# Performance work log

Hardware: AMD Instinct MI355X
Metric: run time of the kernel (lower is better)

The kernel has to match this reference:

```python
import jax, jax.numpy as jnp
import numpy as np

N_NODES = 50000
N_EDGES = 1600000
D_IN = 1028
D_OUT = 256
NEG_SLOPE = 0.2


def setup_inputs() -> dict:
    key = jax.random.key(0)
    ks = jax.random.split(key, 6)
    x = jax.random.normal(ks[0], (N_NODES, D_IN), dtype=jnp.float32)
    edge_index = jax.random.randint(ks[1], (2, N_EDGES), 0, N_NODES, dtype=jnp.int64)
    # GATv2Conv params (heads=1): separate source/target linear maps, attention vector, bias
    W_l = jax.random.normal(ks[2], (D_IN, D_OUT), dtype=jnp.float32) / np.sqrt(D_IN)
    W_r = jax.random.normal(ks[3], (D_IN, D_OUT), dtype=jnp.float32) / np.sqrt(D_IN)
    att = jax.random.normal(ks[4], (D_OUT,), dtype=jnp.float32) / np.sqrt(D_OUT)
    bias = jax.random.normal(ks[5], (D_OUT,), dtype=jnp.float32) * 0.01
    return {"x": x, "edge_index": edge_index, "W_l": W_l, "W_r": W_r, "att": att, "bias": bias}


def reference(x, edge_index, W_l, W_r, att, bias):
    # Single-layer GATv2Conv(1028 -> 256, heads=1, add_self_loops=True)
    n = x.shape[0]
    xl = x @ W_l  # source-side features [N, D_OUT]
    xr = x @ W_r  # target-side features [N, D_OUT]
    loops = jnp.arange(n, dtype=edge_index.dtype)
    src = jnp.concatenate([edge_index[0], loops])  # [E + N]
    dst = jnp.concatenate([edge_index[1], loops])
    # e_ij = a . LeakyReLU(xl[j] + xr[i])
    e = jax.nn.leaky_relu(xl[src] + xr[dst], NEG_SLOPE) @ att  # [E + N]
    # softmax over incoming edges per destination node (self-loops guarantee nonempty segments)
    emax = jax.ops.segment_max(e, dst, num_segments=n)
    p = jnp.exp(e - emax[dst])
    denom = jax.ops.segment_sum(p, dst, num_segments=n)
    alpha = p / denom[dst]  # [E + N]
    out = jax.ops.segment_sum(alpha[:, None] * xl[src], dst, num_segments=n)
    return out + bias
```

## Files before the change

### kernel.cpp

```cpp
#include <hip/hip_runtime.h>
#include <hip/hip_bf16.h>
#include <stdint.h>


#define N_NODES 50000
#define N_EDGES 1600000
#define D_IN    1028
#define KPAD    1056
#define D_OUT   256
#define NB      512

#define X2B_GS     2048
#define X2B_TOT    (N_NODES * 264)
#define WT_TILES   (33 * 8)
#define HIST_GS    1024
#define PREP_BLOCKS (X2B_GS + WT_TILES + HIST_GS)
#define SCAT_GS    2048

typedef __bf16 bf16x8 __attribute__((ext_vector_type(8)));
typedef float  f32x4  __attribute__((ext_vector_type(4)));

static __device__ __forceinline__ void gl_lds16(const void* g, void* l) {
  __builtin_amdgcn_global_load_lds(
      (const __attribute__((address_space(1))) unsigned int*)g,
      (__attribute__((address_space(3))) unsigned int*)l, 16, 0, 0);
}
static __device__ __forceinline__ float bf2f(unsigned short u) {
  union { unsigned int i; float f; } c; c.i = ((unsigned int)u) << 16; return c.f;
}
static __device__ __forceinline__ unsigned short f2bf(float f) {
  union { float f; unsigned int i; } c; c.f = f;
  unsigned int r = 0x7fffu + ((c.i >> 16) & 1u);
  return (unsigned short)((c.i + r) >> 16);
}

__global__ void k_mode(const unsigned int* __restrict__ ei32, int* __restrict__ mode) {
  int t = blockIdx.x * 256 + threadIdx.x;
  if (t < 2048 && ei32[2 * t + 1] != 0u) atomicOr(mode, 1);
}

static __device__ __forceinline__ int load_idx(const int* ei, int md, int pos, int n) {
  int v = md ? ei[pos] : (int)((const long long*)ei)[pos];
  return v < 0 ? 0 : (v >= n ? n - 1 : v);
}

__global__ __launch_bounds__(256) void k_prep(const float* __restrict__ x,
    const float* __restrict__ Wl, const float* __restrict__ Wr,
    const int* __restrict__ ei, const int* __restrict__ mode,
    unsigned short* __restrict__ xb, unsigned short* __restrict__ Wt,
    int* __restrict__ deg) {
  __shared__ unsigned short tile[32][66];
  const int b = blockIdx.x, t = threadIdx.x;
  if (b < X2B_GS) {
    const int TH = X2B_GS * 256;
    for (int c = b * 256 + t; c < X2B_TOT; c += 4 * TH) {
      int cc[4], rw[4], qq[4]; float4 v[4]; bool ld[4];
#pragma unroll
      for (int u = 0; u < 4; ++u) {
        cc[u] = c + u * TH;
        ld[u] = false; rw[u] = 0; qq[u] = 0;
        if (cc[u] < X2B_TOT) {
          rw[u] = cc[u] / 264;
          qq[u] = cc[u] - rw[u] * 264;
          if (qq[u] < 257) {
            v[u] = *(const float4*)(x + (size_t)rw[u] * D_IN + 4 * qq[u]);
            ld[u] = true;
          }
        }
      }
#pragma unroll
      for (int u = 0; u < 4; ++u) {
        if (cc[u] < X2B_TOT) {
          ushort4 o = {0, 0, 0, 0};
          if (ld[u]) { o.x = f2bf(v[u].x); o.y = f2bf(v[u].y);
                       o.z = f2bf(v[u].z); o.w = f2bf(v[u].w); }
          *(ushort4*)(xb + (size_t)rw[u] * KPAD + 4 * qq[u]) = o;
        }
      }
    }
  } else if (b < X2B_GS + WT_TILES) {
    const int w = b - X2B_GS;
    const int k0 = (w >> 3) * 32, n0 = (w & 7) * 64;
#pragma unroll
    for (int j = 0; j < 8; ++j) {
      int k = 4 * j + (t >> 6), n = t & 63;
      unsigned short val = 0;
      if (k0 + k < D_IN) {
        int gn = n0 + n;
        val = f2bf(gn < D_OUT ? Wl[(size_t)(k0 + k) * D_OUT + gn]
                              : Wr[(size_t)(k0 + k) * D_OUT + (gn - D_OUT)]);
      }
      tile[k][n] = val;
    }
    __syncthreads();
#pragma unroll
    for (int j = 0; j < 8; ++j) {
      int n = 8 * j + (t >> 5), k = t & 31;
      Wt[(size_t)(n0 + n) * KPAD + k0 + k] = tile[k][n];
    }
  } else {
    const int md = *mode;
    const int TH = HIST_GS * 256;
    for (int e = (b - X2B_GS - WT_TILES) * 256 + t; e < N_EDGES; e += TH) {
      int d = load_idx(ei, md, N_EDGES + e, N_NODES);
      atomicAdd(&deg[d], 1);
    }
  }
}

__global__ __launch_bounds__(256) void k_gemm(const unsigned short* __restrict__ xb,
                                              const unsigned short* __restrict__ Wt,
                                              unsigned short* __restrict__ xf, int M) {
  __shared__ unsigned short smem[16896];
  unsigned short* As = smem;
  unsigned short* Bs = smem + 4096;
  unsigned short* Cs = smem;
  const int tid = threadIdx.x;
  const int w = tid >> 6, lane = tid & 63;
  const int m0 = blockIdx.x * 128, n0 = blockIdx.y * 128;
  const int wm = (w >> 1) * 64, wn = (w & 1) * 64;

  f32x4 zero = {0.f, 0.f, 0.f, 0.f};
  f32x4 acc[4][4];
#pragma unroll
  for (int i = 0; i < 4; ++i)
#pragma unroll
    for (int j = 0; j < 4; ++j) acc[i][j] = zero;

  const int lrow = lane >> 2, lch = lane & 3;

  for (int k0 = 0; k0 < KPAD; k0 += 32) {
    __syncthreads();
#pragma unroll
    for (int j = 0; j < 2; ++j) {
      int gm = m0 + w * 32 + j * 16 + lrow;
      if (gm >= M) gm = M - 1;
      const char* g = (const char*)xb + ((size_t)gm * KPAD + k0) * 2 + lch * 16;
      gl_lds16(g, &As[(w * 32 + j * 16) * 32]);
    }
#pragma unroll
    for (int j = 0; j < 2; ++j) {
      int gn = n0 + w * 32 + j * 16 + lrow;
      const char* g = (const char*)Wt + ((size_t)gn * KPAD + k0) * 2 + lch * 16;
      gl_lds16(g, &Bs[(w * 32 + j * 16) * 32]);
    }
    __syncthreads();

    bf16x8 af[4], bfr[4];
#pragma unroll
    for (int t = 0; t < 4; ++t)
      af[t] = *(const bf16x8*)&As[(wm + t * 16 + (lane & 15)) * 32 + (lane >> 4) * 8];
#pragma unroll
    for (int t = 0; t < 4; ++t)
      bfr[t] = *(const bf16x8*)&Bs[(wn + t * 16 + (lane & 15)) * 32 + (lane >> 4) * 8];
#pragma unroll
    for (int mt = 0; mt < 4; ++mt)
#pragma unroll
      for (int nt = 0; nt < 4; ++nt)
        acc[mt][nt] = __builtin_amdgcn_mfma_f32_16x16x32_bf16(af[mt], bfr[nt], acc[mt][nt], 0, 0, 0);
  }

  __syncthreads();
  {
    const int col = lane & 15, rq = (lane >> 4) * 4;
#pragma unroll
    for (int mt = 0; mt < 4; ++mt)
#pragma unroll
      for (int nt = 0; nt < 4; ++nt)
#pragma unroll
        for (int r = 0; r < 4; ++r)
          Cs[(wm + mt * 16 + rq + r) * 132 + wn + nt * 16 + col] = f2bf(acc[mt][nt][r]);
  }
  __syncthreads();
  {
    const int row = tid >> 1, half = tid & 1;
    int gm = m0 + row;
    if (gm < M) {
      unsigned short* dst = xf + (size_t)gm * NB + n0 + half * 64;
      const unsigned short* srcp = &Cs[row * 132 + half * 64];
#pragma unroll
      for (int j = 0; j < 8; ++j)
        *(uint4*)(dst + j * 8) = *(const uint4*)(srcp + j * 8);
    }
  }
}

__global__ __launch_bounds__(1024) void k_scan(const int* __restrict__ deg,
    int* __restrict__ rowstart, int* __restrict__ cursor, int n) {
  const int t = (int)threadIdx.x;
  const int lane = t & 63, wid = t >> 6;
  const int seg = (n + 1023) / 1024;
  const int base = t * seg;
  __shared__ int wsum[16];

  int sum = 0;
  for (int j = 0; j < seg; ++j) { int i = base + j; if (i < n) sum += deg[i]; }

  int x = sum;
#pragma unroll
  for (int off = 1; off < 64; off <<= 1) {
    int y = __shfl_up(x, off, 64);
    if (lane >= off) x += y;
  }
  if (lane == 63) wsum[wid] = x;
  __syncthreads();
  if (t < 16) {
    int v = wsum[t], s = v;
#pragma unroll
    for (int off = 1; off < 16; off <<= 1) {
      int y = __shfl_up(s, off, 16);
      if (t >= off) s += y;
    }
    wsum[t] = s - v;
  }
  __syncthreads();
  int run = wsum[wid] + (x - sum);
  for (int j = 0; j < seg; ++j) {
    int i = base + j;
    if (i < n) { rowstart[i] = run; cursor[i] = run; run += deg[i]; }
  }
  if (t == 1023) rowstart[n] = run;
}

__global__ __launch_bounds__(256) void k_scatter(const int* __restrict__ ei,
                          const int* __restrict__ mode,
                          int* __restrict__ cursor, int* __restrict__ ssrc) {
  const int md = *mode;
  const int TH = SCAT_GS * 256;
  for (int e = (int)blockIdx.x * 256 + (int)threadIdx.x; e < N_EDGES; e += TH) {
    int s = load_idx(ei, md, e, N_NODES);
    int d = load_idx(ei, md, N_EDGES + e, N_NODES);
    int pos = atomicAdd(&cursor[d], 1);
    if (pos >= 0 && pos < N_EDGES) ssrc[pos] = s;
  }
}

static __device__ __forceinline__ void unpack8(uint4 u, float* v) {
  union { unsigned int i; float f; } c;
  c.i = u.x << 16;         v[0] = c.f;
  c.i = u.x & 0xffff0000u; v[1] = c.f;
  c.i = u.y << 16;         v[2] = c.f;
  c.i = u.y & 0xffff0000u; v[3] = c.f;
  c.i = u.z << 16;         v[4] = c.f;
  c.i = u.z & 0xffff0000u; v[5] = c.f;
  c.i = u.w << 16;         v[6] = c.f;
  c.i = u.w & 0xffff0000u; v[7] = c.f;
}
static __device__ __forceinline__ float dot8(const float* v, const float* xr, const float* a) {
  float e = 0.f;
#pragma unroll
  for (int d = 0; d < 8; ++d) {
    float t = v[d] + xr[d];
    t = fmaxf(t, 0.2f * t);
    e = fmaf(a[d], t, e);
  }
  return e;
}
static __device__ __forceinline__ float red32(float e) {
#pragma unroll
  for (int off = 1; off < 32; off <<= 1) e += __shfl_xor(e, off, 64);
  return e;
}

__global__ __launch_bounds__(256) void k_gat(const unsigned short* __restrict__ xf,
    const int* __restrict__ rowstart, const int* __restrict__ ssrc,
    const float* __restrict__ att, const float* __restrict__ bias,
    float* __restrict__ out, int n) {
  const int gw = (int)blockIdx.x * 4 + (int)(threadIdx.x >> 6);
  const int lane = (int)(threadIdx.x & 63);
  const int grp = lane >> 5, gl = lane & 31;
  if (gw >= n) return;

  float a[8];
  {
    float4 A0 = ((const float4*)att)[2 * gl];
    float4 A1 = ((const float4*)att)[2 * gl + 1];
    a[0] = A0.x; a[1] = A0.y; a[2] = A0.z; a[3] = A0.w;
    a[4] = A1.x; a[5] = A1.y; a[6] = A1.z; a[7] = A1.w;
  }
  float xr[8], vs[8];
  unpack8(*(const uint4*)(xf + (size_t)gw * NB + D_OUT + 8 * gl), xr);
  unpack8(*(const uint4*)(xf + (size_t)gw * NB + 8 * gl), vs);

  float m, l, acc[8];
  {
    float e = red32(dot8(vs, xr, a));
    if (grp == 0) {
      m = e; l = 1.f;
#pragma unroll
      for (int d = 0; d < 8; ++d) acc[d] = vs[d];
    } else {
      m = -1e30f; l = 0.f;
#pragma unroll
      for (int d = 0; d < 8; ++d) acc[d] = 0.f;
    }
  }

  const int end = rowstart[gw + 1];
  int i = rowstart[gw] + grp;
  bool have = i < end;
  uint4 vu;
  if (have) {
    unsigned s = (unsigned)ssrc[i];
    vu = *(const uint4*)(xf + ((size_t)s << 9) + 8 * gl);
  }
  while (have) {
    int i2 = i + 2;
    bool have2 = i2 < end;
    uint4 vu2;
    if (have2) {
      unsigned s2 = (unsigned)ssrc[i2];
      vu2 = *(const uint4*)(xf + ((size_t)s2 << 9) + 8 * gl);
    }
    float v[8];
    unpack8(vu, v);
    float e = red32(dot8(v, xr, a));
    float mn = fmaxf(m, e);
    float sc = __expf(m - mn);
    float p  = __expf(e - mn);
#pragma unroll
    for (int d = 0; d < 8; ++d) acc[d] = fmaf(p, v[d], acc[d] * sc);
    l = fmaf(l, sc, p);
    m = mn;
    vu = vu2; i = i2; have = have2;
  }

  float mo = __shfl_xor(m, 32, 64);
  float mM = fmaxf(m, mo);
  float sA = __expf(m - mM);
  float lA = l * sA;
  float lS = lA + __shfl_xor(lA, 32, 64);
  float inv = 1.f / lS;
#pragma unroll
  for (int d = 0; d < 8; ++d) {
    float t = acc[d] * sA;
    acc[d] = t + __shfl_xor(t, 32, 64);
  }
  if (grp == 0) {
    float4 B0 = ((const float4*)bias)[2 * gl];
    float4 B1 = ((const float4*)bias)[2 * gl + 1];
    float4 o0, o1;
    o0.x = fmaf(acc[0], inv, B0.x); o0.y = fmaf(acc[1], inv, B0.y);
    o0.z = fmaf(acc[2], inv, B0.z); o0.w = fmaf(acc[3], inv, B0.w);
    o1.x = fmaf(acc[4], inv, B1.x); o1.y = fmaf(acc[5], inv, B1.y);
    o1.z = fmaf(acc[6], inv, B1.z); o1.w = fmaf(acc[7], inv, B1.w);
    ((float4*)out)[(size_t)gw * 64 + 2 * gl] = o0;
    ((float4*)out)[(size_t)gw * 64 + 2 * gl + 1] = o1;
  }
}

extern "C" void kernel_launch(void* const* d_in, const int* in_sizes, int n_in,
                              void* d_out, int out_size, void* d_ws, size_t ws_size,
                              hipStream_t stream) {
  (void)in_sizes; (void)n_in; (void)out_size; (void)ws_size;
  const float* x   = (const float*)d_in[0];
  const int*   ei  = (const int*)d_in[1];
  const float* Wl  = (const float*)d_in[2];
  const float* Wr  = (const float*)d_in[3];
  const float* att = (const float*)d_in[4];
  const float* bia = (const float*)d_in[5];
  float* out = (float*)d_out;

  const int N = N_NODES;
  const int E = N_EDGES;

  char* ws = (char*)d_ws;
  size_t off = 0;
  unsigned short* xb = (unsigned short*)(ws + off); off += (size_t)N * KPAD * 2;
  unsigned short* xf = (unsigned short*)(ws + off); off += (size_t)N * NB * 2;
  unsigned short* Wt = (unsigned short*)(ws + off); off += (size_t)NB * KPAD * 2;
  off = (off + 255) & ~(size_t)255;
  int* deg      = (int*)(ws + off); off += (size_t)N * 4;
  int* mode     = (int*)(ws + off); off += 256;
  int* rowstart = (int*)(ws + off); off += (size_t)(N + 1) * 4;
  off = (off + 255) & ~(size_t)255;
  int* cursor   = (int*)(ws + off); off += (size_t)N * 4;
  int* ssrc     = (int*)(ws + off); off += (size_t)E * 4;

  hipMemsetAsync(deg, 0, (size_t)N * 4 + 256, stream);
  k_mode<<<8, 256, 0, stream>>>((const unsigned int*)ei, mode);
  k_prep<<<PREP_BLOCKS, 256, 0, stream>>>(x, Wl, Wr, ei, mode, xb, Wt, deg);
  k_gemm<<<dim3((N + 127) / 128, NB / 128), 256, 0, stream>>>(xb, Wt, xf, N);
  k_scan<<<1, 1024, 0, stream>>>(deg, rowstart, cursor, N);
  k_scatter<<<SCAT_GS, 256, 0, stream>>>(ei, mode, cursor, ssrc);
  k_gat<<<(N + 3) / 4, 256, 0, stream>>>(xf, rowstart, ssrc, att, bia, out, N);
}
```

Before: 847.0 us.

## Fuse fp32-to-bf16 conversion of x into GEMM A-tile loads

Removes the separate pass that converted x to a padded bf16 buffer. The GEMM now reads fp32 x directly, converts it in registers with packed bf16 conversion instructions, and stores the result to LDS. The grid is also swapped so the N-tile blocks of the same M rows run next to each other, which should help the repeated fp32 x reads hit in cache. This saves writing and re-reading about 100MB of intermediate data. In exchange the GEMM's A loads are twice as wide, go through registers instead of direct-to-LDS, and each x row is read once per N tile (four times).

```diff
diff --git a/kernel.cpp b/kernel.cpp
--- a/kernel.cpp
+++ b/kernel.cpp
@@ -10,11 +10,9 @@
 #define D_OUT   256
 #define NB      512
 
-#define X2B_GS     2048
-#define X2B_TOT    (N_NODES * 264)
 #define WT_TILES   (33 * 8)
 #define HIST_GS    1024
-#define PREP_BLOCKS (X2B_GS + WT_TILES + HIST_GS)
+#define PREP_BLOCKS (WT_TILES + HIST_GS)
 #define SCAT_GS    2048
 
 typedef __bf16 bf16x8 __attribute__((ext_vector_type(8)));
@@ -25,14 +23,16 @@
       (const __attribute__((address_space(1))) unsigned int*)g,
       (__attribute__((address_space(3))) unsigned int*)l, 16, 0, 0);
 }
-static __device__ __forceinline__ float bf2f(unsigned short u) {
-  union { unsigned int i; float f; } c; c.i = ((unsigned int)u) << 16; return c.f;
-}
 static __device__ __forceinline__ unsigned short f2bf(float f) {
   union { float f; unsigned int i; } c; c.f = f;
   unsigned int r = 0x7fffu + ((c.i >> 16) & 1u);
   return (unsigned short)((c.i + r) >> 16);
 }
+static __device__ __forceinline__ unsigned int cvt_pk_bf16(float lo, float hi) {
+  unsigned int r;
+  asm("v_cvt_pk_bf16_f32 %0, %1, %2" : "=v"(r) : "v"(lo), "v"(hi));
+  return r;
+}
 
 __global__ void k_mode(const unsigned int* __restrict__ ei32, int* __restrict__ mode) {
   int t = blockIdx.x * 256 + threadIdx.x;
@@ -44,43 +44,14 @@
   return v < 0 ? 0 : (v >= n ? n - 1 : v);
 }
 
-__global__ __launch_bounds__(256) void k_prep(const float* __restrict__ x,
-    const float* __restrict__ Wl, const float* __restrict__ Wr,
-    const int* __restrict__ ei, const int* __restrict__ mode,
-    unsigned short* __restrict__ xb, unsigned short* __restrict__ Wt,
+__global__ __launch_bounds__(256) void k_prep(const float* __restrict__ Wl,
+    const float* __restrict__ Wr, const int* __restrict__ ei,
+    const int* __restrict__ mode, unsigned short* __restrict__ Wt,
     int* __restrict__ deg) {
   __shared__ unsigned short tile[32][66];
   const int b = blockIdx.x, t = threadIdx.x;
-  if (b < X2B_GS) {
-    const int TH = X2B_GS * 256;
-    for (int c = b * 256 + t; c < X2B_TOT; c += 4 * TH) {
-      int cc[4], rw[4], qq[4]; float4 v[4]; bool ld[4];
-#pragma unroll
-      for (int u = 0; u < 4; ++u) {
-        cc[u] = c + u * TH;
-        ld[u] = false; rw[u] = 0; qq[u] = 0;
-        if (cc[u] < X2B_TOT) {
-          rw[u] = cc[u] / 264;
-          qq[u] = cc[u] - rw[u] * 264;
-          if (qq[u] < 257) {
-            v[u] = *(const float4*)(x + (size_t)rw[u] * D_IN + 4 * qq[u]);
-            ld[u] = true;
-          }
-        }
-      }
-#pragma unroll
-      for (int u = 0; u < 4; ++u) {
-        if (cc[u] < X2B_TOT) {
-          ushort4 o = {0, 0, 0, 0};
-          if (ld[u]) { o.x = f2bf(v[u].x); o.y = f2bf(v[u].y);
-                       o.z = f2bf(v[u].z); o.w = f2bf(v[u].w); }
-          *(ushort4*)(xb + (size_t)rw[u] * KPAD + 4 * qq[u]) = o;
-        }
-      }
-    }
-  } else if (b < X2B_GS + WT_TILES) {
-    const int w = b - X2B_GS;
-    const int k0 = (w >> 3) * 32, n0 = (w & 7) * 64;
+  if (b < WT_TILES) {
+    const int k0 = (b >> 3) * 32, n0 = (b & 7) * 64;
 #pragma unroll
     for (int j = 0; j < 8; ++j) {
       int k = 4 * j + (t >> 6), n = t & 63;
@@ -101,14 +72,14 @@
   } else {
     const int md = *mode;
     const int TH = HIST_GS * 256;
-    for (int e = (b - X2B_GS - WT_TILES) * 256 + t; e < N_EDGES; e += TH) {
+    for (int e = (b - WT_TILES) * 256 + t; e < N_EDGES; e += TH) {
       int d = load_idx(ei, md, N_EDGES + e, N_NODES);
       atomicAdd(&deg[d], 1);
     }
   }
 }
 
-__global__ __launch_bounds__(256) void k_gemm(const unsigned short* __restrict__ xb,
+__global__ __launch_bounds__(256) void k_gemm(const float* __restrict__ x,
                                               const unsigned short* __restrict__ Wt,
                                               unsigned short* __restrict__ xf, int M) {
   __shared__ unsigned short smem[16896];
@@ -117,7 +88,7 @@
   unsigned short* Cs = smem;
   const int tid = threadIdx.x;
   const int w = tid >> 6, lane = tid & 63;
-  const int m0 = blockIdx.x * 128, n0 = blockIdx.y * 128;
+  const int m0 = blockIdx.y * 128, n0 = blockIdx.x * 128;
   const int wm = (w >> 1) * 64, wn = (w & 1) * 64;
 
   f32x4 zero = {0.f, 0.f, 0.f, 0.f};
@@ -131,18 +102,30 @@
 
   for (int k0 = 0; k0 < KPAD; k0 += 32) {
     __syncthreads();
+    float4 f[4];
+    int gka = k0 + lch * 8;
 #pragma unroll
     for (int j = 0; j < 2; ++j) {
       int gm = m0 + w * 32 + j * 16 + lrow;
       if (gm >= M) gm = M - 1;
-      const char* g = (const char*)xb + ((size_t)gm * KPAD + k0) * 2 + lch * 16;
-      gl_lds16(g, &As[(w * 32 + j * 16) * 32]);
+      const float* gp = x + (size_t)gm * D_IN + gka;
+      f[2 * j]     = (gka     < D_IN) ? *(const float4*)gp       : *(const float4*)&zero;
+      f[2 * j + 1] = (gka + 4 < D_IN) ? *(const float4*)(gp + 4) : *(const float4*)&zero;
     }
 #pragma unroll
     for (int j = 0; j < 2; ++j) {
       int gn = n0 + w * 32 + j * 16 + lrow;
       const char* g = (const char*)Wt + ((size_t)gn * KPAD + k0) * 2 + lch * 16;
       gl_lds16(g, &Bs[(w * 32 + j * 16) * 32]);
+    }
+#pragma unroll
+    for (int j = 0; j < 2; ++j) {
+      uint4 pk;
+      pk.x = cvt_pk_bf16(f[2 * j].x,     f[2 * j].y);
+      pk.y = cvt_pk_bf16(f[2 * j].z,     f[2 * j].w);
+      pk.z = cvt_pk_bf16(f[2 * j + 1].x, f[2 * j + 1].y);
+      pk.w = cvt_pk_bf16(f[2 * j + 1].z, f[2 * j + 1].w);
+      *(uint4*)&As[(w * 32 + j * 16 + lrow) * 32 + lch * 8] = pk;
     }
     __syncthreads();
 
@@ -366,7 +349,6 @@
 
   char* ws = (char*)d_ws;
   size_t off = 0;
-  unsigned short* xb = (unsigned short*)(ws + off); off += (size_t)N * KPAD * 2;
   unsigned short* xf = (unsigned short*)(ws + off); off += (size_t)N * NB * 2;
   unsigned short* Wt = (unsigned short*)(ws + off); off += (size_t)NB * KPAD * 2;
   off = (off + 255) & ~(size_t)255;
@@ -379,8 +361,8 @@
 
   hipMemsetAsync(deg, 0, (size_t)N * 4 + 256, stream);
   k_mode<<<8, 256, 0, stream>>>((const unsigned int*)ei, mode);
-  k_prep<<<PREP_BLOCKS, 256, 0, stream>>>(x, Wl, Wr, ei, mode, xb, Wt, deg);
-  k_gemm<<<dim3((N + 127) / 128, NB / 128), 256, 0, stream>>>(xb, Wt, xf, N);
+  k_prep<<<PREP_BLOCKS, 256, 0, stream>>>(Wl, Wr, ei, mode, Wt, deg);
+  k_gemm<<<dim3(NB / 128, (N + 127) / 128), 256, 0, stream>>>(x, Wt, xf, N);
   k_scan<<<1, 1024, 0, stream>>>(deg, rowstart, cursor, N);
   k_scatter<<<SCAT_GS, 256, 0, stream>>>(ei, mode, cursor, ssrc);
   k_gat<<<(N + 3) / 4, 256, 0, stream>>>(xf, rowstart, ssrc, att, bia, out, N);
```

New measurement: 1.046 ms. +23.5%, slower.

## Merge edge scatter into GEMM launch and branch online-softmax update

Applied to the files above, without the earlier changes.

Moves k_scan ahead of the GEMM and folds the CSR edge scatter into the GEMM kernel as extra blocks on a 1-D grid. Scatter and GEMM now run concurrently, overlapping the atomic-heavy, memory-bound scatter with the compute-bound matmul and removing one launch. The GAT online-softmax loop also now branches on whether the new score exceeds the running max, so each edge needs only one exp instead of two. The branch can diverge across lanes, and the scatter blocks compete with GEMM blocks for CU slots.

```diff
diff --git a/kernel.cpp b/kernel.cpp
--- a/kernel.cpp
+++ b/kernel.cpp
@@ -15,7 +15,11 @@
 #define WT_TILES   (33 * 8)
 #define HIST_GS    1024
 #define PREP_BLOCKS (X2B_GS + WT_TILES + HIST_GS)
-#define SCAT_GS    2048
+
+#define M_TILES 391
+#define GEMM_MN (M_TILES * 4)
+#define SCAT_B  2048
+#define GS_BLOCKS (GEMM_MN + SCAT_B)
 
 typedef __bf16 bf16x8 __attribute__((ext_vector_type(8)));
 typedef float  f32x4  __attribute__((ext_vector_type(4)));
@@ -24,9 +28,6 @@
   __builtin_amdgcn_global_load_lds(
       (const __attribute__((address_space(1))) unsigned int*)g,
       (__attribute__((address_space(3))) unsigned int*)l, 16, 0, 0);
-}
-static __device__ __forceinline__ float bf2f(unsigned short u) {
-  union { unsigned int i; float f; } c; c.i = ((unsigned int)u) << 16; return c.f;
 }
 static __device__ __forceinline__ unsigned short f2bf(float f) {
   union { float f; unsigned int i; } c; c.f = f;
@@ -109,15 +110,28 @@
 }
 
 __global__ __launch_bounds__(256) void k_gemm(const unsigned short* __restrict__ xb,
-                                              const unsigned short* __restrict__ Wt,
-                                              unsigned short* __restrict__ xf, int M) {
+    const unsigned short* __restrict__ Wt, unsigned short* __restrict__ xf, int M,
+    const int* __restrict__ ei, const int* __restrict__ mode,
+    int* __restrict__ cursor, int* __restrict__ ssrc) {
+  const int bid = (int)blockIdx.x;
+  if (bid >= GEMM_MN) {
+    const int md = *mode;
+    const int TH = SCAT_B * 256;
+    for (int e = (bid - GEMM_MN) * 256 + (int)threadIdx.x; e < N_EDGES; e += TH) {
+      int s = load_idx(ei, md, e, N_NODES);
+      int d = load_idx(ei, md, N_EDGES + e, N_NODES);
+      int pos = atomicAdd(&cursor[d], 1);
+      if (pos >= 0 && pos < N_EDGES) ssrc[pos] = s;
+    }
+    return;
+  }
   __shared__ unsigned short smem[16896];
   unsigned short* As = smem;
   unsigned short* Bs = smem + 4096;
   unsigned short* Cs = smem;
   const int tid = threadIdx.x;
   const int w = tid >> 6, lane = tid & 63;
-  const int m0 = blockIdx.x * 128, n0 = blockIdx.y * 128;
+  const int m0 = (bid % M_TILES) * 128, n0 = (bid / M_TILES) * 128;
   const int wm = (w >> 1) * 64, wn = (w & 1) * 64;
 
   f32x4 zero = {0.f, 0.f, 0.f, 0.f};
@@ -220,19 +234,6 @@
     if (i < n) { rowstart[i] = run; cursor[i] = run; run += deg[i]; }
   }
   if (t == 1023) rowstart[n] = run;
-}
-
-__global__ __launch_bounds__(256) void k_scatter(const int* __restrict__ ei,
-                          const int* __restrict__ mode,
-                          int* __restrict__ cursor, int* __restrict__ ssrc) {
-  const int md = *mode;
-  const int TH = SCAT_GS * 256;
-  for (int e = (int)blockIdx.x * 256 + (int)threadIdx.x; e < N_EDGES; e += TH) {
-    int s = load_idx(ei, md, e, N_NODES);
-    int d = load_idx(ei, md, N_EDGES + e, N_NODES);
-    int pos = atomicAdd(&cursor[d], 1);
-    if (pos >= 0 && pos < N_EDGES) ssrc[pos] = s;
-  }
 }
 
 static __device__ __forceinline__ void unpack8(uint4 u, float* v) {
@@ -315,13 +316,18 @@
     float v[8];
     unpack8(vu, v);
     float e = red32(dot8(v, xr, a));
-    float mn = fmaxf(m, e);
-    float sc = __expf(m - mn);
-    float p  = __expf(e - mn);
-#pragma unroll
-    for (int d = 0; d < 8; ++d) acc[d] = fmaf(p, v[d], acc[d] * sc);
-    l = fmaf(l, sc, p);
-    m = mn;
+    if (e <= m) {
+      float p = __expf(e - m);
+#pragma unroll
+      for (int d = 0; d < 8; ++d) acc[d] = fmaf(p, v[d], acc[d]);
+      l += p;
+    } else {
+      float sc = __expf(m - e);
+#pragma unroll
+      for (int d = 0; d < 8; ++d) acc[d] = fmaf(acc[d], sc, v[d]);
+      l = fmaf(l, sc, 1.f);
+      m = e;
+    }
     vu = vu2; i = i2; have = have2;
   }
 
@@ -380,8 +386,7 @@
   hipMemsetAsync(deg, 0, (size_t)N * 4 + 256, stream);
   k_mode<<<8, 256, 0, stream>>>((const unsigned int*)ei, mode);
   k_prep<<<PREP_BLOCKS, 256, 0, stream>>>(x, Wl, Wr, ei, mode, xb, Wt, deg);
-  k_gemm<<<dim3((N + 127) / 128, NB / 128), 256, 0, stream>>>(xb, Wt, xf, N);
   k_scan<<<1, 1024, 0, stream>>>(deg, rowstart, cursor, N);
-  k_scatter<<<SCAT_GS, 256, 0, stream>>>(ei, mode, cursor, ssrc);
+  k_gemm<<<GS_BLOCKS, 256, 0, stream>>>(xb, Wt, xf, N, ei, mode, cursor, ssrc);
   k_gat<<<(N + 3) / 4, 256, 0, stream>>>(xf, rowstart, ssrc, att, bia, out, N);
 }
```

New measurement: 830.7 us. No clear change (-1.9%).
